# Performance work log

Measured on AMD Instinct MI355X. Metric: run time of the kernel, lower is better.

The kernel has to match this reference:

```python
import math
import jax, jax.numpy as jnp
import numpy as np

EMBED_DIM = 1024
NUM_HEADS = 16
HEAD_DIM = EMBED_DIM // NUM_HEADS


def _xavier(key, fan_in, fan_out):
    lim = math.sqrt(6.0 / (fan_in + fan_out))
    return jax.random.uniform(key, (fan_out, fan_in), jnp.float32, -lim, lim)


def setup_inputs() -> dict:
    key = jax.random.key(0)
    kx, kq, kk, kv, ko = jax.random.split(key, 5)
    B, L = 4, 2048
    x = jax.random.normal(kx, (B, L, EMBED_DIM), jnp.float32)
    return {
        "x": x,
        "wq": _xavier(kq, EMBED_DIM, EMBED_DIM), "bq": jnp.zeros((EMBED_DIM,), jnp.float32),
        "wk": _xavier(kk, EMBED_DIM, EMBED_DIM), "bk": jnp.zeros((EMBED_DIM,), jnp.float32),
        "wv": _xavier(kv, EMBED_DIM, EMBED_DIM), "bv": jnp.zeros((EMBED_DIM,), jnp.float32),
        "wo": _xavier(ko, EMBED_DIM, EMBED_DIM), "bo": jnp.zeros((EMBED_DIM,), jnp.float32),
    }


def reference(x, wq, bq, wk, bk, wv, bv, wo, bo):
    B, L, D = x.shape
    H, Dh = NUM_HEADS, HEAD_DIM

    def proj(w, b):
        # nn.Linear: x @ w.T + b, then split heads -> (B, H, L, Dh)
        return (jnp.einsum('bld,ed->ble', x, w) + b).reshape(B, L, H, Dh).transpose(0, 2, 1, 3)

    q, k, v = proj(wq, bq), proj(wk, bk), proj(wv, bv)
    # NOTE: original torch code scales by sqrt(key.size(dim=1)) == sqrt(num_heads)
    scale = 1.0 / math.sqrt(H)
    scores = jnp.einsum('bhqd,bhkd->bhqk', q, k) * scale  # (B, H, L, L)
    attn = jax.nn.softmax(scores, axis=-1)
    out = jnp.einsum('bhqk,bhkd->bhqd', attn, v)          # (B, H, L, Dh)
    out = out.transpose(0, 2, 1, 3).reshape(B, L, D)
    return jnp.einsum('bld,ed->ble', out, wo) + bo
```

## Files before the change

### kernel.cpp

```cpp
#include <hip/hip_runtime.h>
#include <hip/hip_bf16.h>

#define DEVI __device__ __forceinline__

using u16 = unsigned short;
typedef __attribute__((ext_vector_type(8))) short bf16x8;
typedef __attribute__((ext_vector_type(4))) short bf16x4;
typedef __attribute__((ext_vector_type(4))) float f32x4;

constexpr int Bb = 4, Ls = 2048, Dd = 1024, Hh = 16, DhC = 64;
constexpr int Mm = Bb * Ls;

DEVI u16 f2bf(float f) {
  union { float f; unsigned u; } x; x.f = f;
  unsigned r = x.u + 0x7FFFu + ((x.u >> 16) & 1u);
  return (u16)(r >> 16);
}
DEVI float bf2f(u16 b) {
  union { unsigned u; float f; } x; x.u = ((unsigned)b) << 16;
  return x.f;
}

DEVI unsigned cvt_pk_bf16(float a, float b) {
  unsigned d;
  asm("v_cvt_pk_bf16_f32 %0, %1, %2" : "=v"(d) : "v"(a), "v"(b));
  return d;
}

DEVI void gload_lds16(const u16* g, u16* l) {
  __builtin_amdgcn_global_load_lds(
      (const __attribute__((address_space(1))) unsigned int*)g,
      (__attribute__((address_space(3))) unsigned int*)l, 16, 0, 0);
}

DEVI bf16x8 ld_frag(const u16* p) { return *reinterpret_cast<const bf16x8*>(p); }

__global__ void cvt_all(const float* __restrict__ x,
                        const float* __restrict__ wq, const float* __restrict__ wk,
                        const float* __restrict__ wv, const float* __restrict__ wo,
                        u16* __restrict__ xb,
                        u16* __restrict__ wqb, u16* __restrict__ wkb,
                        u16* __restrict__ wvb, u16* __restrict__ wob) {
  const int tid = blockIdx.x * blockDim.x + threadIdx.x;
  constexpr int NT = 2048 * 256;
  constexpr int N4X = Mm * Dd / 4;
  constexpr int N4W = Dd * Dd / 4;
  for (int i = tid; i < N4X; i += NT) {
    float4 v = reinterpret_cast<const float4*>(x)[i];
    reinterpret_cast<ushort4*>(xb)[i] =
        make_ushort4(f2bf(v.x), f2bf(v.y), f2bf(v.z), f2bf(v.w));
  }
  for (int i = tid; i < 4 * N4W; i += NT) {
    int which = i / N4W, off = i - which * N4W;
    const float* s = which == 0 ? wq : which == 1 ? wk : which == 2 ? wv : wo;
    u16* d = which == 0 ? wqb : which == 1 ? wkb : which == 2 ? wvb : wob;
    float4 v = reinterpret_cast<const float4*>(s)[off];
    reinterpret_cast<ushort4*>(d)[off] =
        make_ushort4(f2bf(v.x), f2bf(v.y), f2bf(v.z), f2bf(v.w));
  }
}

__global__ __launch_bounds__(512) void gemm_qkv(
    const u16* __restrict__ A, const u16* __restrict__ W,
    const float* __restrict__ bq, const float* __restrict__ bk2,
    const float* __restrict__ bv,
    u16* __restrict__ qm, u16* __restrict__ km, u16* __restrict__ vt)
{
  constexpr int K = 1024, BK = 64, NSTEP = K / BK;
  __shared__ u16 ldsA[2][128 * 64];
  __shared__ u16 ldsB[2][256 * 64];

  const int tid = threadIdx.x;
  const int wave = tid >> 6, lane = tid & 63;
  const int wr = wave >> 2, wc = wave & 3;
  const int lrow = lane & 15, hi = lane >> 4, lk = hi * 8;
  const int swz = (lrow & 7) << 3;

  const int lin = blockIdx.y * 12 + blockIdx.x;
  const int nid = (lin & 7) * 96 + (lin >> 3);
  const int bx = nid % 12, by = nid / 12;
  const int m0 = by * 128;
  const int n0g = bx * 256;

  int a_row[2], a_kc[2], b_row[4], b_kc[4];
#pragma unroll
  for (int g = 0; g < 2; ++g) {
    int c = g * 512 + tid;
    a_row[g] = c >> 3;
    a_kc[g] = ((c & 7) ^ (a_row[g] & 7)) * 8;
  }
#pragma unroll
  for (int g = 0; g < 4; ++g) {
    int c = g * 512 + tid;
    b_row[g] = c >> 3;
    b_kc[g] = ((c & 7) ^ (b_row[g] & 7)) * 8;
  }

  f32x4 acc[4][4] = {};

#pragma unroll
  for (int g = 0; g < 2; ++g)
    gload_lds16(A + (size_t)(m0 + a_row[g]) * K + a_kc[g], &ldsA[0][0] + (g * 512 + tid) * 8);
#pragma unroll
  for (int g = 0; g < 4; ++g)
    gload_lds16(W + (size_t)(n0g + b_row[g]) * K + b_kc[g], &ldsB[0][0] + (g * 512 + tid) * 8);
  __syncthreads();

  for (int t = 0; t < NSTEP; ++t) {
    const u16* Ab = &ldsA[t & 1][0];
    const u16* Bb = &ldsB[t & 1][0];
    u16* An = &ldsA[(t + 1) & 1][0];
    u16* Bn = &ldsB[(t + 1) & 1][0];
    const int k1 = (t + 1) * BK;
    const bool more = (t + 1 < NSTEP);

    bf16x8 a[4][2], b0[2][2], b1[2][2];

#pragma unroll
    for (int f = 0; f < 4; ++f) {
      int row = wr * 64 + f * 16 + lrow;
      a[f][0] = ld_frag(Ab + row * 64 + (lk ^ swz));
      a[f][1] = ld_frag(Ab + row * 64 + ((32 + lk) ^ swz));
    }
#pragma unroll
    for (int f = 0; f < 2; ++f) {
      int row = wc * 64 + f * 16 + lrow;
      b0[f][0] = ld_frag(Bb + row * 64 + (lk ^ swz));
      b0[f][1] = ld_frag(Bb + row * 64 + ((32 + lk) ^ swz));
    }
    if (more) {
      gload_lds16(A + (size_t)(m0 + a_row[0]) * K + k1 + a_kc[0], An + (0 * 512 + tid) * 8);
      gload_lds16(A + (size_t)(m0 + a_row[1]) * K + k1 + a_kc[1], An + (1 * 512 + tid) * 8);
      gload_lds16(W + (size_t)(n0g + b_row[0]) * K + k1 + b_kc[0], Bn + (0 * 512 + tid) * 8);
    }
    __builtin_amdgcn_s_barrier();
    __builtin_amdgcn_s_setprio(1);
#pragma unroll
    for (int fm = 0; fm < 4; ++fm)
#pragma unroll
      for (int fn = 0; fn < 2; ++fn)
#pragma unroll
        for (int kk = 0; kk < 2; ++kk)
          acc[fm][fn] = __builtin_amdgcn_mfma_f32_16x16x32_bf16(a[fm][kk], b0[fn][kk], acc[fm][fn], 0, 0, 0);
    __builtin_amdgcn_s_setprio(0);
    __builtin_amdgcn_s_barrier();

#pragma unroll
    for (int f = 0; f < 2; ++f) {
      int row = wc * 64 + (2 + f) * 16 + lrow;
      b1[f][0] = ld_frag(Bb + row * 64 + (lk ^ swz));
      b1[f][1] = ld_frag(Bb + row * 64 + ((32 + lk) ^ swz));
    }
    if (more) {
      gload_lds16(W + (size_t)(n0g + b_row[1]) * K + k1 + b_kc[1], Bn + (1 * 512 + tid) * 8);
      gload_lds16(W + (size_t)(n0g + b_row[2]) * K + k1 + b_kc[2], Bn + (2 * 512 + tid) * 8);
      gload_lds16(W + (size_t)(n0g + b_row[3]) * K + k1 + b_kc[3], Bn + (3 * 512 + tid) * 8);
    }
    __builtin_amdgcn_s_barrier();
    __builtin_amdgcn_s_setprio(1);
#pragma unroll
    for (int fm = 0; fm < 4; ++fm)
#pragma unroll
      for (int fn = 0; fn < 2; ++fn)
#pragma unroll
        for (int kk = 0; kk < 2; ++kk)
          acc[fm][2 + fn] = __builtin_amdgcn_mfma_f32_16x16x32_bf16(a[fm][kk], b1[fn][kk], acc[fm][2 + fn], 0, 0, 0);
    __builtin_amdgcn_s_setprio(0);
    if (more) asm volatile("s_waitcnt vmcnt(0)" ::: "memory");
    __builtin_amdgcn_s_barrier();
  }

  const int region = bx >> 2;
  const int nc0 = (bx & 3) * 256;
  const float* bias = region == 0 ? bq : region == 1 ? bk2 : bv;
  u16* dstRM = region == 0 ? qm : km;

#pragma unroll
  for (int fm = 0; fm < 4; ++fm) {
#pragma unroll
    for (int fn = 0; fn < 4; ++fn) {
      int row = m0 + wr * 64 + fm * 16 + hi * 4;
      int col = nc0 + wc * 64 + fn * 16 + lrow;
      float bv_ = bias[col];
      if (region == 2) {
        ushort4 o;
        o.x = f2bf(acc[fm][fn][0] + bv_); o.y = f2bf(acc[fm][fn][1] + bv_);
        o.z = f2bf(acc[fm][fn][2] + bv_); o.w = f2bf(acc[fm][fn][3] + bv_);
        *reinterpret_cast<ushort4*>(&vt[(size_t)col * Mm + row]) = o;
      } else {
#pragma unroll
        for (int j = 0; j < 4; ++j)
          dstRM[(size_t)(row + j) * Dd + col] = f2bf(acc[fm][fn][j] + bv_);
      }
    }
  }
}

__global__ __launch_bounds__(256) void gemm_out(
    const u16* __restrict__ A, const u16* __restrict__ Bt,
    const float* __restrict__ bias, float* __restrict__ C, int M, int N, int K)
{
  constexpr int BK = 64;
  __shared__ u16 As[128 * BK];
  __shared__ u16 Bs[128 * BK];
  const int tid = threadIdx.x;
  const int wave = tid >> 6, lane = tid & 63;
  const int wr = wave >> 1, wc = wave & 1;
  const int lrow = lane & 15, lk = (lane >> 4) * 8;
  const int m0 = blockIdx.y * 128, n0 = blockIdx.x * 128;
  const int srow = lane >> 3, scol = (lane & 7) * 8;

  f32x4 acc[4][4] = {};

  for (int k0 = 0; k0 < K; k0 += BK) {
    __syncthreads();
#pragma unroll
    for (int i = 0; i < 4; ++i) {
      int g = wave * 4 + i;
      int row = g * 8 + srow;
      gload_lds16(A  + (size_t)(m0 + row) * K + k0 + scol, As + g * 512);
      gload_lds16(Bt + (size_t)(n0 + row) * K + k0 + scol, Bs + g * 512);
    }
    __syncthreads();
#pragma unroll
    for (int kk = 0; kk < 2; ++kk) {
      bf16x8 af[4], bfr[4];
#pragma unroll
      for (int m = 0; m < 4; ++m) af[m]  = ld_frag(As + (wr*64 + m*16 + lrow)*BK + kk*32 + lk);
#pragma unroll
      for (int n = 0; n < 4; ++n) bfr[n] = ld_frag(Bs + (wc*64 + n*16 + lrow)*BK + kk*32 + lk);
      __builtin_amdgcn_s_setprio(1);
#pragma unroll
      for (int m = 0; m < 4; ++m)
#pragma unroll
        for (int n = 0; n < 4; ++n)
          acc[m][n] = __builtin_amdgcn_mfma_f32_16x16x32_bf16(af[m], bfr[n], acc[m][n], 0, 0, 0);
      __builtin_amdgcn_s_setprio(0);
    }
  }

#pragma unroll
  for (int m = 0; m < 4; ++m) {
#pragma unroll
    for (int n = 0; n < 4; ++n) {
      int row = m0 + wr*64 + m*16 + (lane >> 4) * 4;
      int col = n0 + wc*64 + n*16 + lrow;
      float bv = bias[col];
#pragma unroll
      for (int j = 0; j < 4; ++j)
        C[(size_t)(row + j) * N + col] = acc[m][n][j] + bv;
    }
  }
}

__global__ __launch_bounds__(512) void attn_fwd(
    const u16* __restrict__ Qm, const u16* __restrict__ Km,
    const u16* __restrict__ Vt, u16* __restrict__ Om)
{
  __shared__ u16 Ks[2][4096];
  __shared__ u16 Vs[2][4096];

  const int tid = threadIdx.x;
  const int wave = tid >> 6, lane = tid & 63;
  const int lrow = lane & 15, lk = (lane >> 4) * 8;
  const int swz = (lrow & 7) << 3;
  const int b = blockIdx.x >> 4, h = blockIdx.x & 15;
  const int rb = b * Ls;
  const int cb0 = h * DhC;
  const int q0 = blockIdx.y * 128;
  const int srow = lane >> 3;
  const int scol = ((lane & 7) ^ srow) * 8;

  const u16* kg = Km + (size_t)(rb + wave * 8 + srow) * Dd + cb0 + scol;
  const u16* vg = Vt + (size_t)(cb0 + wave * 8 + srow) * Mm + rb + scol;
  u16* ksflat = &Ks[0][0];
  u16* vsflat = &Vs[0][0];
  u16* ksl = ksflat + wave * 512;
  u16* vsl = vsflat + wave * 512;
  constexpr int LBUF = 4096;

#pragma unroll
  for (int g = 0; g < 2; ++g)
    gload_lds16(Qm + (size_t)(rb + q0 + wave * 16 + g * 8 + srow) * Dd + cb0 + scol,
                ksflat + (wave * 2 + g) * 512);
  gload_lds16(vg, vsl);
  __syncthreads();

  constexpr float SCL = 0.25f * 1.44269504088896f;
  bf16x8 aq0 = ld_frag(ksflat + (wave * 16 + lrow) * 64 + (lk ^ swz));
  bf16x8 aq1 = ld_frag(ksflat + (wave * 16 + lrow) * 64 + ((32 + lk) ^ swz));
#pragma unroll
  for (int e = 0; e < 8; e += 2) {
    unsigned d0 = cvt_pk_bf16(SCL * bf2f((u16)aq0[e]), SCL * bf2f((u16)aq0[e + 1]));
    unsigned d1 = cvt_pk_bf16(SCL * bf2f((u16)aq1[e]), SCL * bf2f((u16)aq1[e + 1]));
    aq0[e] = (short)(d0 & 0xffff); aq0[e + 1] = (short)(d0 >> 16);
    aq1[e] = (short)(d1 & 0xffff); aq1[e + 1] = (short)(d1 >> 16);
  }
  __syncthreads();
  gload_lds16(kg, ksl);
  __syncthreads();

  bf16x8 ones;
#pragma unroll
  for (int e = 0; e < 8; ++e) ones[e] = (short)0x3F80;

  f32x4 accO[4] = {};
  f32x4 acc_ps = {};

  int nb = 0;
  for (int kv0 = 0; kv0 < Ls; kv0 += 64) {
    if (kv0 + 64 < Ls) {
      int dst = (nb ^ 1) * LBUF;
      gload_lds16(kg + (size_t)(kv0 + 64) * Dd, ksl + dst);
      gload_lds16(vg + kv0 + 64, vsl + dst);
      asm volatile("s_waitcnt vmcnt(2)" ::: "memory");
    } else {
      asm volatile("s_waitcnt vmcnt(0)" ::: "memory");
    }
    __builtin_amdgcn_s_barrier();
    const u16* ks = ksflat + nb * LBUF;
    const u16* vs = vsflat + nb * LBUF;

    f32x4 s[4];
#pragma unroll
    for (int kb = 0; kb < 4; ++kb) {
      const u16* kr = ks + (kb * 16 + lrow) * 64;
      bf16x8 bk0 = ld_frag(kr + (lk ^ swz));
      bf16x8 bk1 = ld_frag(kr + ((32 + lk) ^ swz));
      f32x4 t = {};
      __builtin_amdgcn_s_setprio(1);
      t = __builtin_amdgcn_mfma_f32_16x16x32_bf16(bk0, aq0, t, 0, 0, 0);
      t = __builtin_amdgcn_mfma_f32_16x16x32_bf16(bk1, aq1, t, 0, 0, 0);
      __builtin_amdgcn_s_setprio(0);
      s[kb] = t;
    }

    unsigned u00 = cvt_pk_bf16(__builtin_amdgcn_exp2f(s[0][0]), __builtin_amdgcn_exp2f(s[0][1]));
    unsigned u01 = cvt_pk_bf16(__builtin_amdgcn_exp2f(s[0][2]), __builtin_amdgcn_exp2f(s[0][3]));
    unsigned u10 = cvt_pk_bf16(__builtin_amdgcn_exp2f(s[1][0]), __builtin_amdgcn_exp2f(s[1][1]));
    unsigned u11 = cvt_pk_bf16(__builtin_amdgcn_exp2f(s[1][2]), __builtin_amdgcn_exp2f(s[1][3]));
    unsigned u20 = cvt_pk_bf16(__builtin_amdgcn_exp2f(s[2][0]), __builtin_amdgcn_exp2f(s[2][1]));
    unsigned u21 = cvt_pk_bf16(__builtin_amdgcn_exp2f(s[2][2]), __builtin_amdgcn_exp2f(s[2][3]));
    unsigned u30 = cvt_pk_bf16(__builtin_amdgcn_exp2f(s[3][0]), __builtin_amdgcn_exp2f(s[3][1]));
    unsigned u31 = cvt_pk_bf16(__builtin_amdgcn_exp2f(s[3][2]), __builtin_amdgcn_exp2f(s[3][3]));

    asm("v_permlane32_swap_b32 %0, %1" : "+v"(u00), "+v"(u10));
    asm("v_permlane16_swap_b32 %0, %1" : "+v"(u00), "+v"(u10));
    asm("v_permlane32_swap_b32 %0, %1" : "+v"(u01), "+v"(u11));
    asm("v_permlane16_swap_b32 %0, %1" : "+v"(u01), "+v"(u11));
    asm("v_permlane32_swap_b32 %0, %1" : "+v"(u20), "+v"(u30));
    asm("v_permlane16_swap_b32 %0, %1" : "+v"(u20), "+v"(u30));
    asm("v_permlane32_swap_b32 %0, %1" : "+v"(u21), "+v"(u31));
    asm("v_permlane16_swap_b32 %0, %1" : "+v"(u21), "+v"(u31));

    union { unsigned u[4]; bf16x8 v; } apc0, apc1;
    apc0.u[0] = u00; apc0.u[1] = u01; apc0.u[2] = u10; apc0.u[3] = u11;
    apc1.u[0] = u20; apc1.u[1] = u21; apc1.u[2] = u30; apc1.u[3] = u31;

#pragma unroll
    for (int kk2 = 0; kk2 < 2; ++kk2) {
      bf16x8 ap = kk2 == 0 ? apc0.v : apc1.v;
      __builtin_amdgcn_s_setprio(1);
#pragma unroll
      for (int cb = 0; cb < 4; ++cb) {
        const u16* vr = vs + (cb * 16 + lrow) * 64;
        bf16x8 bv = ld_frag(vr + ((kk2 * 32 + lk) ^ swz));
        accO[cb] = __builtin_amdgcn_mfma_f32_16x16x32_bf16(bv, ap, accO[cb], 0, 0, 0);
      }
      acc_ps = __builtin_amdgcn_mfma_f32_16x16x32_bf16(ones, ap, acc_ps, 0, 0, 0);
      __builtin_amdgcn_s_setprio(0);
    }

    if (kv0 + 64 < Ls) __builtin_amdgcn_s_barrier();
    nb ^= 1;
  }

  float rinv = 1.0f / acc_ps[0];
  const size_t orow = (size_t)(rb + q0 + wave * 16 + lrow) * Dd + cb0;
#pragma unroll
  for (int cb = 0; cb < 4; ++cb) {
    uint2 o;
    o.x = cvt_pk_bf16(accO[cb][0] * rinv, accO[cb][1] * rinv);
    o.y = cvt_pk_bf16(accO[cb][2] * rinv, accO[cb][3] * rinv);
    *reinterpret_cast<uint2*>(&Om[orow + cb * 16 + (lk >> 1)]) = o;
  }
}

extern "C" void kernel_launch(void* const* d_in, const int* in_sizes, int n_in,
                              void* d_out, int out_size, void* d_ws, size_t ws_size,
                              hipStream_t stream) {
  (void)in_sizes; (void)n_in; (void)out_size; (void)ws_size;
  const float* x  = (const float*)d_in[0];
  const float* wq = (const float*)d_in[1];
  const float* bq = (const float*)d_in[2];
  const float* wk = (const float*)d_in[3];
  const float* bk = (const float*)d_in[4];
  const float* wv = (const float*)d_in[5];
  const float* bv = (const float*)d_in[6];
  const float* wo = (const float*)d_in[7];
  const float* bo = (const float*)d_in[8];
  float* out = (float*)d_out;

  u16* ws  = (u16*)d_ws;
  u16* xb  = ws;
  u16* wqb = xb  + (size_t)Mm * Dd;
  u16* wkb = wqb + (size_t)Dd * Dd;
  u16* wvb = wkb + (size_t)Dd * Dd;
  u16* wob = wvb + (size_t)Dd * Dd;
  u16* qm  = wob + (size_t)Dd * Dd;
  u16* km  = qm  + (size_t)Mm * Dd;
  u16* vt  = km  + (size_t)Mm * Dd;
  u16* om  = xb;

  cvt_all<<<2048, 256, 0, stream>>>(x, wq, wk, wv, wo, xb, wqb, wkb, wvb, wob);

  dim3 qkvgrid(3 * Dd / 256, Mm / 128);
  gemm_qkv<<<qkvgrid, 512, 0, stream>>>(xb, wqb, bq, bk, bv, qm, km, vt);

  dim3 agrid(Bb * Hh, Ls / 128);
  attn_fwd<<<agrid, 512, 0, stream>>>(qm, km, vt, om);

  dim3 ogrid(Dd / 128, Mm / 128);
  gemm_out<<<ogrid, 256, 0, stream>>>(om, wob, bo, out, Mm, Dd, Dd);
}
```

Baseline: 194.0 us.

## Double query rows per attention wave and pipeline the output-projection GEMM

The attention kernel now gives each wave 32 query rows instead of 16. Each K fragment loaded from LDS is reused across two QK^T MFMA sets and each V fragment across two PV sets, which halves the grid and the K/V global traffic per query. The output GEMM is rewritten as a 512-thread, 128x256-tile kernel with double-buffered swizzled LDS, prefetch loads split across two half-steps, and an XCD-aware block remap. The costs are higher register pressure, fewer blocks for occupancy in attention, and extra LDS in the GEMM.

```diff
diff --git a/kernel.cpp b/kernel.cpp
--- a/kernel.cpp
+++ b/kernel.cpp
@@ -196,59 +196,124 @@
   }
 }
 
-__global__ __launch_bounds__(256) void gemm_out(
+__global__ __launch_bounds__(512) void gemm_out(
     const u16* __restrict__ A, const u16* __restrict__ Bt,
-    const float* __restrict__ bias, float* __restrict__ C, int M, int N, int K)
+    const float* __restrict__ bias, float* __restrict__ C)
 {
-  constexpr int BK = 64;
-  __shared__ u16 As[128 * BK];
-  __shared__ u16 Bs[128 * BK];
+  constexpr int K = 1024, N = 1024, BK = 64, NSTEP = K / BK;
+  __shared__ u16 ldsA[2][128 * 64];
+  __shared__ u16 ldsB[2][256 * 64];
+
   const int tid = threadIdx.x;
   const int wave = tid >> 6, lane = tid & 63;
-  const int wr = wave >> 1, wc = wave & 1;
-  const int lrow = lane & 15, lk = (lane >> 4) * 8;
-  const int m0 = blockIdx.y * 128, n0 = blockIdx.x * 128;
-  const int srow = lane >> 3, scol = (lane & 7) * 8;
+  const int wr = wave >> 2, wc = wave & 3;
+  const int lrow = lane & 15, hi = lane >> 4, lk = hi * 8;
+  const int swz = (lrow & 7) << 3;
+
+  const int lin = blockIdx.y * 4 + blockIdx.x;
+  const int nid = (lin & 7) * 32 + (lin >> 3);
+  const int bx = nid % 4, by = nid / 4;
+  const int m0 = by * 128;
+  const int n0 = bx * 256;
+
+  int a_row[2], a_kc[2], b_row[4], b_kc[4];
+#pragma unroll
+  for (int g = 0; g < 2; ++g) {
+    int c = g * 512 + tid;
+    a_row[g] = c >> 3;
+    a_kc[g] = ((c & 7) ^ (a_row[g] & 7)) * 8;
+  }
+#pragma unroll
+  for (int g = 0; g < 4; ++g) {
+    int c = g * 512 + tid;
+    b_row[g] = c >> 3;
+    b_kc[g] = ((c & 7) ^ (b_row[g] & 7)) * 8;
+  }
 
   f32x4 acc[4][4] = {};
 
-  for (int k0 = 0; k0 < K; k0 += BK) {
-    __syncthreads();
-#pragma unroll
-    for (int i = 0; i < 4; ++i) {
-      int g = wave * 4 + i;
-      int row = g * 8 + srow;
-      gload_lds16(A  + (size_t)(m0 + row) * K + k0 + scol, As + g * 512);
-      gload_lds16(Bt + (size_t)(n0 + row) * K + k0 + scol, Bs + g * 512);
-    }
-    __syncthreads();
-#pragma unroll
-    for (int kk = 0; kk < 2; ++kk) {
-      bf16x8 af[4], bfr[4];
-#pragma unroll
-      for (int m = 0; m < 4; ++m) af[m]  = ld_frag(As + (wr*64 + m*16 + lrow)*BK + kk*32 + lk);
-#pragma unroll
-      for (int n = 0; n < 4; ++n) bfr[n] = ld_frag(Bs + (wc*64 + n*16 + lrow)*BK + kk*32 + lk);
-      __builtin_amdgcn_s_setprio(1);
-#pragma unroll
-      for (int m = 0; m < 4; ++m)
-#pragma unroll
-        for (int n = 0; n < 4; ++n)
-          acc[m][n] = __builtin_amdgcn_mfma_f32_16x16x32_bf16(af[m], bfr[n], acc[m][n], 0, 0, 0);
-      __builtin_amdgcn_s_setprio(0);
-    }
-  }
-
-#pragma unroll
-  for (int m = 0; m < 4; ++m) {
-#pragma unroll
-    for (int n = 0; n < 4; ++n) {
-      int row = m0 + wr*64 + m*16 + (lane >> 4) * 4;
-      int col = n0 + wc*64 + n*16 + lrow;
+#pragma unroll
+  for (int g = 0; g < 2; ++g)
+    gload_lds16(A + (size_t)(m0 + a_row[g]) * K + a_kc[g], &ldsA[0][0] + (g * 512 + tid) * 8);
+#pragma unroll
+  for (int g = 0; g < 4; ++g)
+    gload_lds16(Bt + (size_t)(n0 + b_row[g]) * K + b_kc[g], &ldsB[0][0] + (g * 512 + tid) * 8);
+  __syncthreads();
+
+  for (int t = 0; t < NSTEP; ++t) {
+    const u16* Ab = &ldsA[t & 1][0];
+    const u16* Bb = &ldsB[t & 1][0];
+    u16* An = &ldsA[(t + 1) & 1][0];
+    u16* Bn = &ldsB[(t + 1) & 1][0];
+    const int k1 = (t + 1) * BK;
+    const bool more = (t + 1 < NSTEP);
+
+    bf16x8 a[4][2], b0[2][2], b1[2][2];
+
+#pragma unroll
+    for (int f = 0; f < 4; ++f) {
+      int row = wr * 64 + f * 16 + lrow;
+      a[f][0] = ld_frag(Ab + row * 64 + (lk ^ swz));
+      a[f][1] = ld_frag(Ab + row * 64 + ((32 + lk) ^ swz));
+    }
+#pragma unroll
+    for (int f = 0; f < 2; ++f) {
+      int row = wc * 64 + f * 16 + lrow;
+      b0[f][0] = ld_frag(Bb + row * 64 + (lk ^ swz));
+      b0[f][1] = ld_frag(Bb + row * 64 + ((32 + lk) ^ swz));
+    }
+    if (more) {
+      gload_lds16(A + (size_t)(m0 + a_row[0]) * K + k1 + a_kc[0], An + (0 * 512 + tid) * 8);
+      gload_lds16(A + (size_t)(m0 + a_row[1]) * K + k1 + a_kc[1], An + (1 * 512 + tid) * 8);
+      gload_lds16(Bt + (size_t)(n0 + b_row[0]) * K + k1 + b_kc[0], Bn + (0 * 512 + tid) * 8);
+    }
+    __builtin_amdgcn_s_barrier();
+    __builtin_amdgcn_s_setprio(1);
+#pragma unroll
+    for (int fm = 0; fm < 4; ++fm)
+#pragma unroll
+      for (int fn = 0; fn < 2; ++fn)
+#pragma unroll
+        for (int kk = 0; kk < 2; ++kk)
+          acc[fm][fn] = __builtin_amdgcn_mfma_f32_16x16x32_bf16(a[fm][kk], b0[fn][kk], acc[fm][fn], 0, 0, 0);
+    __builtin_amdgcn_s_setprio(0);
+    __builtin_amdgcn_s_barrier();
+
+#pragma unroll
+    for (int f = 0; f < 2; ++f) {
+      int row = wc * 64 + (2 + f) * 16 + lrow;
+      b1[f][0] = ld_frag(Bb + row * 64 + (lk ^ swz));
+      b1[f][1] = ld_frag(Bb + row * 64 + ((32 + lk) ^ swz));
+    }
+    if (more) {
+      gload_lds16(Bt + (size_t)(n0 + b_row[1]) * K + k1 + b_kc[1], Bn + (1 * 512 + tid) * 8);
+      gload_lds16(Bt + (size_t)(n0 + b_row[2]) * K + k1 + b_kc[2], Bn + (2 * 512 + tid) * 8);
+      gload_lds16(Bt + (size_t)(n0 + b_row[3]) * K + k1 + b_kc[3], Bn + (3 * 512 + tid) * 8);
+    }
+    __builtin_amdgcn_s_barrier();
+    __builtin_amdgcn_s_setprio(1);
+#pragma unroll
+    for (int fm = 0; fm < 4; ++fm)
+#pragma unroll
+      for (int fn = 0; fn < 2; ++fn)
+#pragma unroll
+        for (int kk = 0; kk < 2; ++kk)
+          acc[fm][2 + fn] = __builtin_amdgcn_mfma_f32_16x16x32_bf16(a[fm][kk], b1[fn][kk], acc[fm][2 + fn], 0, 0, 0);
+    __builtin_amdgcn_s_setprio(0);
+    if (more) asm volatile("s_waitcnt vmcnt(0)" ::: "memory");
+    __builtin_amdgcn_s_barrier();
+  }
+
+#pragma unroll
+  for (int fm = 0; fm < 4; ++fm) {
+#pragma unroll
+    for (int fn = 0; fn < 4; ++fn) {
+      int row = m0 + wr * 64 + fm * 16 + hi * 4;
+      int col = n0 + wc * 64 + fn * 16 + lrow;
       float bv = bias[col];
 #pragma unroll
       for (int j = 0; j < 4; ++j)
-        C[(size_t)(row + j) * N + col] = acc[m][n][j] + bv;
+        C[(size_t)(row + j) * N + col] = acc[fm][fn][j] + bv;
     }
   }
 }
@@ -267,7 +332,7 @@
   const int b = blockIdx.x >> 4, h = blockIdx.x & 15;
   const int rb = b * Ls;
   const int cb0 = h * DhC;
-  const int q0 = blockIdx.y * 128;
+  const int q0 = blockIdx.y * 256;
   const int srow = lane >> 3;
   const int scol = ((lane & 7) ^ srow) * 8;
 
@@ -280,32 +345,63 @@
   constexpr int LBUF = 4096;
 
 #pragma unroll
-  for (int g = 0; g < 2; ++g)
-    gload_lds16(Qm + (size_t)(rb + q0 + wave * 16 + g * 8 + srow) * Dd + cb0 + scol,
-                ksflat + (wave * 2 + g) * 512);
-  gload_lds16(vg, vsl);
+  for (int g = 0; g < 4; ++g) {
+    int c = wave * 4 + g;
+    u16* dst = c < 16 ? ksflat + c * 512 : vsflat + (c - 16) * 512;
+    gload_lds16(Qm + (size_t)(rb + q0 + c * 8 + srow) * Dd + cb0 + scol, dst);
+  }
   __syncthreads();
 
   constexpr float SCL = 0.25f * 1.44269504088896f;
-  bf16x8 aq0 = ld_frag(ksflat + (wave * 16 + lrow) * 64 + (lk ^ swz));
-  bf16x8 aq1 = ld_frag(ksflat + (wave * 16 + lrow) * 64 + ((32 + lk) ^ swz));
-#pragma unroll
-  for (int e = 0; e < 8; e += 2) {
-    unsigned d0 = cvt_pk_bf16(SCL * bf2f((u16)aq0[e]), SCL * bf2f((u16)aq0[e + 1]));
-    unsigned d1 = cvt_pk_bf16(SCL * bf2f((u16)aq1[e]), SCL * bf2f((u16)aq1[e + 1]));
-    aq0[e] = (short)(d0 & 0xffff); aq0[e + 1] = (short)(d0 >> 16);
-    aq1[e] = (short)(d1 & 0xffff); aq1[e + 1] = (short)(d1 >> 16);
+  bf16x8 aq[2][2];
+#pragma unroll
+  for (int t = 0; t < 2; ++t) {
+    int row = wave * 32 + t * 16 + lrow;
+    const u16* base = row < 128 ? ksflat + row * 64 : vsflat + (row - 128) * 64;
+    aq[t][0] = ld_frag(base + (lk ^ swz));
+    aq[t][1] = ld_frag(base + ((32 + lk) ^ swz));
+#pragma unroll
+    for (int e = 0; e < 8; e += 2) {
+      unsigned d0 = cvt_pk_bf16(SCL * bf2f((u16)aq[t][0][e]), SCL * bf2f((u16)aq[t][0][e + 1]));
+      unsigned d1 = cvt_pk_bf16(SCL * bf2f((u16)aq[t][1][e]), SCL * bf2f((u16)aq[t][1][e + 1]));
+      aq[t][0][e] = (short)(d0 & 0xffff); aq[t][0][e + 1] = (short)(d0 >> 16);
+      aq[t][1][e] = (short)(d1 & 0xffff); aq[t][1][e + 1] = (short)(d1 >> 16);
+    }
   }
   __syncthreads();
   gload_lds16(kg, ksl);
-  __syncthreads();
+  gload_lds16(vg, vsl);
 
   bf16x8 ones;
 #pragma unroll
   for (int e = 0; e < 8; ++e) ones[e] = (short)0x3F80;
 
-  f32x4 accO[4] = {};
-  f32x4 acc_ps = {};
+  f32x4 accO[2][4] = {};
+  f32x4 acc_ps[2] = {};
+
+#define SM_PACK(SIN, AP0, AP1)                                                 \
+  {                                                                            \
+    unsigned u00 = cvt_pk_bf16(__builtin_amdgcn_exp2f(SIN[0][0]), __builtin_amdgcn_exp2f(SIN[0][1])); \
+    unsigned u01 = cvt_pk_bf16(__builtin_amdgcn_exp2f(SIN[0][2]), __builtin_amdgcn_exp2f(SIN[0][3])); \
+    unsigned u10 = cvt_pk_bf16(__builtin_amdgcn_exp2f(SIN[1][0]), __builtin_amdgcn_exp2f(SIN[1][1])); \
+    unsigned u11 = cvt_pk_bf16(__builtin_amdgcn_exp2f(SIN[1][2]), __builtin_amdgcn_exp2f(SIN[1][3])); \
+    unsigned u20 = cvt_pk_bf16(__builtin_amdgcn_exp2f(SIN[2][0]), __builtin_amdgcn_exp2f(SIN[2][1])); \
+    unsigned u21 = cvt_pk_bf16(__builtin_amdgcn_exp2f(SIN[2][2]), __builtin_amdgcn_exp2f(SIN[2][3])); \
+    unsigned u30 = cvt_pk_bf16(__builtin_amdgcn_exp2f(SIN[3][0]), __builtin_amdgcn_exp2f(SIN[3][1])); \
+    unsigned u31 = cvt_pk_bf16(__builtin_amdgcn_exp2f(SIN[3][2]), __builtin_amdgcn_exp2f(SIN[3][3])); \
+    asm("v_permlane32_swap_b32 %0, %1" : "+v"(u00), "+v"(u10));                \
+    asm("v_permlane16_swap_b32 %0, %1" : "+v"(u00), "+v"(u10));                \
+    asm("v_permlane32_swap_b32 %0, %1" : "+v"(u01), "+v"(u11));                \
+    asm("v_permlane16_swap_b32 %0, %1" : "+v"(u01), "+v"(u11));                \
+    asm("v_permlane32_swap_b32 %0, %1" : "+v"(u20), "+v"(u30));                \
+    asm("v_permlane16_swap_b32 %0, %1" : "+v"(u20), "+v"(u30));                \
+    asm("v_permlane32_swap_b32 %0, %1" : "+v"(u21), "+v"(u31));                \
+    asm("v_permlane16_swap_b32 %0, %1" : "+v"(u21), "+v"(u31));                \
+    union { unsigned u[4]; bf16x8 v; } c0_, c1_;                               \
+    c0_.u[0] = u00; c0_.u[1] = u01; c0_.u[2] = u10; c0_.u[3] = u11;            \
+    c1_.u[0] = u20; c1_.u[1] = u21; c1_.u[2] = u30; c1_.u[3] = u31;            \
+    AP0 = c0_.v; AP1 = c1_.v;                                                  \
+  }
 
   int nb = 0;
   for (int kv0 = 0; kv0 < Ls; kv0 += 64) {
@@ -321,68 +417,74 @@
     const u16* ks = ksflat + nb * LBUF;
     const u16* vs = vsflat + nb * LBUF;
 
-    f32x4 s[4];
+    bf16x8 bk[4][2];
 #pragma unroll
     for (int kb = 0; kb < 4; ++kb) {
       const u16* kr = ks + (kb * 16 + lrow) * 64;
-      bf16x8 bk0 = ld_frag(kr + (lk ^ swz));
-      bf16x8 bk1 = ld_frag(kr + ((32 + lk) ^ swz));
-      f32x4 t = {};
+      bk[kb][0] = ld_frag(kr + (lk ^ swz));
+      bk[kb][1] = ld_frag(kr + ((32 + lk) ^ swz));
+    }
+
+    bf16x8 ap0[2], ap1[2];
+
+    {
+      f32x4 s[4];
       __builtin_amdgcn_s_setprio(1);
-      t = __builtin_amdgcn_mfma_f32_16x16x32_bf16(bk0, aq0, t, 0, 0, 0);
-      t = __builtin_amdgcn_mfma_f32_16x16x32_bf16(bk1, aq1, t, 0, 0, 0);
+#pragma unroll
+      for (int kb = 0; kb < 4; ++kb) {
+        f32x4 u = {};
+        u = __builtin_amdgcn_mfma_f32_16x16x32_bf16(bk[kb][0], aq[0][0], u, 0, 0, 0);
+        u = __builtin_amdgcn_mfma_f32_16x16x32_bf16(bk[kb][1], aq[0][1], u, 0, 0, 0);
+        s[kb] = u;
+      }
       __builtin_amdgcn_s_setprio(0);
-      s[kb] = t;
-    }
-
-    unsigned u00 = cvt_pk_bf16(__builtin_amdgcn_exp2f(s[0][0]), __builtin_amdgcn_exp2f(s[0][1]));
-    unsigned u01 = cvt_pk_bf16(__builtin_amdgcn_exp2f(s[0][2]), __builtin_amdgcn_exp2f(s[0][3]));
-    unsigned u10 = cvt_pk_bf16(__builtin_amdgcn_exp2f(s[1][0]), __builtin_amdgcn_exp2f(s[1][1]));
-    unsigned u11 = cvt_pk_bf16(__builtin_amdgcn_exp2f(s[1][2]), __builtin_amdgcn_exp2f(s[1][3]));
-    unsigned u20 = cvt_pk_bf16(__builtin_amdgcn_exp2f(s[2][0]), __builtin_amdgcn_exp2f(s[2][1]));
-    unsigned u21 = cvt_pk_bf16(__builtin_amdgcn_exp2f(s[2][2]), __builtin_amdgcn_exp2f(s[2][3]));
-    unsigned u30 = cvt_pk_bf16(__builtin_amdgcn_exp2f(s[3][0]), __builtin_amdgcn_exp2f(s[3][1]));
-    unsigned u31 = cvt_pk_bf16(__builtin_amdgcn_exp2f(s[3][2]), __builtin_amdgcn_exp2f(s[3][3]));
-
-    asm("v_permlane32_swap_b32 %0, %1" : "+v"(u00), "+v"(u10));
-    asm("v_permlane16_swap_b32 %0, %1" : "+v"(u00), "+v"(u10));
-    asm("v_permlane32_swap_b32 %0, %1" : "+v"(u01), "+v"(u11));
-    asm("v_permlane16_swap_b32 %0, %1" : "+v"(u01), "+v"(u11));
-    asm("v_permlane32_swap_b32 %0, %1" : "+v"(u20), "+v"(u30));
-    asm("v_permlane16_swap_b32 %0, %1" : "+v"(u20), "+v"(u30));
-    asm("v_permlane32_swap_b32 %0, %1" : "+v"(u21), "+v"(u31));
-    asm("v_permlane16_swap_b32 %0, %1" : "+v"(u21), "+v"(u31));
-
-    union { unsigned u[4]; bf16x8 v; } apc0, apc1;
-    apc0.u[0] = u00; apc0.u[1] = u01; apc0.u[2] = u10; apc0.u[3] = u11;
-    apc1.u[0] = u20; apc1.u[1] = u21; apc1.u[2] = u30; apc1.u[3] = u31;
+      SM_PACK(s, ap0[0], ap0[1]);
+    }
+    {
+      f32x4 s[4];
+      __builtin_amdgcn_s_setprio(1);
+#pragma unroll
+      for (int kb = 0; kb < 4; ++kb) {
+        f32x4 u = {};
+        u = __builtin_amdgcn_mfma_f32_16x16x32_bf16(bk[kb][0], aq[1][0], u, 0, 0, 0);
+        u = __builtin_amdgcn_mfma_f32_16x16x32_bf16(bk[kb][1], aq[1][1], u, 0, 0, 0);
+        s[kb] = u;
+      }
+      __builtin_amdgcn_s_setprio(0);
+      SM_PACK(s, ap1[0], ap1[1]);
+    }
 
 #pragma unroll
     for (int kk2 = 0; kk2 < 2; ++kk2) {
-      bf16x8 ap = kk2 == 0 ? apc0.v : apc1.v;
       __builtin_amdgcn_s_setprio(1);
 #pragma unroll
       for (int cb = 0; cb < 4; ++cb) {
         const u16* vr = vs + (cb * 16 + lrow) * 64;
         bf16x8 bv = ld_frag(vr + ((kk2 * 32 + lk) ^ swz));
-        accO[cb] = __builtin_amdgcn_mfma_f32_16x16x32_bf16(bv, ap, accO[cb], 0, 0, 0);
+        accO[0][cb] = __builtin_amdgcn_mfma_f32_16x16x32_bf16(bv, ap0[kk2], accO[0][cb], 0, 0, 0);
+        accO[1][cb] = __builtin_amdgcn_mfma_f32_16x16x32_bf16(bv, ap1[kk2], accO[1][cb], 0, 0, 0);
       }
-      acc_ps = __builtin_amdgcn_mfma_f32_16x16x32_bf16(ones, ap, acc_ps, 0, 0, 0);
+      acc_ps[0] = __builtin_amdgcn_mfma_f32_16x16x32_bf16(ones, ap0[kk2], acc_ps[0], 0, 0, 0);
+      acc_ps[1] = __builtin_amdgcn_mfma_f32_16x16x32_bf16(ones, ap1[kk2], acc_ps[1], 0, 0, 0);
       __builtin_amdgcn_s_setprio(0);
     }
 
     if (kv0 + 64 < Ls) __builtin_amdgcn_s_barrier();
     nb ^= 1;
   }
-
-  float rinv = 1.0f / acc_ps[0];
-  const size_t orow = (size_t)(rb + q0 + wave * 16 + lrow) * Dd + cb0;
-#pragma unroll
-  for (int cb = 0; cb < 4; ++cb) {
-    uint2 o;
-    o.x = cvt_pk_bf16(accO[cb][0] * rinv, accO[cb][1] * rinv);
-    o.y = cvt_pk_bf16(accO[cb][2] * rinv, accO[cb][3] * rinv);
-    *reinterpret_cast<uint2*>(&Om[orow + cb * 16 + (lk >> 1)]) = o;
+#undef SM_PACK
+
+#pragma unroll
+  for (int t = 0; t < 2; ++t) {
+    float rinv = 1.0f / acc_ps[t][0];
+    const size_t orow = (size_t)(rb + q0 + wave * 32 + t * 16 + lrow) * Dd + cb0;
+#pragma unroll
+    for (int cb = 0; cb < 4; ++cb) {
+      uint2 o;
+      o.x = cvt_pk_bf16(accO[t][cb][0] * rinv, accO[t][cb][1] * rinv);
+      o.y = cvt_pk_bf16(accO[t][cb][2] * rinv, accO[t][cb][3] * rinv);
+      *reinterpret_cast<uint2*>(&Om[orow + cb * 16 + (lk >> 1)]) = o;
+    }
   }
 }
 
@@ -417,9 +519,9 @@
   dim3 qkvgrid(3 * Dd / 256, Mm / 128);
   gemm_qkv<<<qkvgrid, 512, 0, stream>>>(xb, wqb, bq, bk, bv, qm, km, vt);
 
-  dim3 agrid(Bb * Hh, Ls / 128);
+  dim3 agrid(Bb * Hh, Ls / 256);
   attn_fwd<<<agrid, 512, 0, stream>>>(qm, km, vt, om);
 
-  dim3 ogrid(Dd / 128, Mm / 128);
-  gemm_out<<<ogrid, 256, 0, stream>>>(om, wob, bo, out, Mm, Dd, Dd);
-}
+  dim3 ogrid(Dd / 256, Mm / 128);
+  gemm_out<<<ogrid, 512, 0, stream>>>(om, wob, bo, out);
+}
```

Result: faster. 177.6 us (-8.4%).
